# Performance work log

Measured on AMD Instinct MI355X. Metric: run time of the kernel, lower is better.

Reference implementation:

```python
import jax, jax.numpy as jnp
import numpy as np

EMB = 512
GP = 128
NH = 8
HD = EMB // NH  # 64
B = 2
S = 1024


def _rel_shift(x):
    # Faithful port of DoubleAttentionLayer._rel_shift (pads dim 1, reinterprets
    # (B, J+1, K, n) as (J+1, B, K, n), drops first slice). Row-major reshape
    # semantics match torch .view on contiguous tensors exactly.
    Bsz, J, K, N = x.shape
    zp = jnp.zeros((Bsz, 1, K, N), x.dtype)
    xp = jnp.concatenate([zp, x], axis=1).reshape(J + 1, Bsz, K, N)
    return xp[1:].reshape(Bsz, J, K, N)


def _layernorm(x):
    # nn.LayerNorm(emb_dim, elementwise_affine=False), eps=1e-5
    m = jnp.mean(x, axis=-1, keepdims=True)
    v = jnp.var(x, axis=-1, keepdims=True)
    return (x - m) / jnp.sqrt(v + 1e-5)


def _attention(q, k, v, Bc, Bp, gpe, mask, Wp_w, Wp_b):
    Bsz, J, E = q.shape
    K = k.shape[1]
    # content scores
    qc = jnp.tanh((q + Bc).reshape(Bsz, J, NH, HD))
    kh = jnp.tanh(k.reshape(Bsz, K, NH, HD))
    ctx = jnp.einsum('bjnd,bknd->bjkn', qc, kh)
    # position scores (tanh before reshape in source for qp -- elementwise, same math)
    qp = jnp.tanh(q + Bp).reshape(Bsz, J, NH, HD)
    kp = jnp.tanh((gpe @ Wp_w + Wp_b).reshape(Bsz, -1, NH, HD))
    pos = jnp.einsum('bjnd,bknd->bjkn', qp, kp)
    pad = ctx.shape[2] - pos.shape[2]  # static; 0 in this configuration
    if pad > 0:
        # replicate-pad pos at front of k dim; constant(0)-pad mask (torch F.pad defaults)
        pos = jnp.concatenate([jnp.broadcast_to(pos[:, :, :1], (Bsz, J, pad, NH)), pos], axis=2)
        mask = jnp.concatenate([jnp.zeros(mask.shape[:2] + (pad, mask.shape[3]), mask.dtype), mask], axis=2)
    pos = _rel_shift(pos)
    att = (ctx + pos) / (HD ** 0.5) - 1e30 * mask
    att = jax.nn.softmax(att, axis=2)
    vh = jnp.tanh(v.reshape(Bsz, K, NH, HD))
    return jnp.einsum('bjkn,bknd->bjnd', att, vh).reshape(Bsz, J, E)


def setup_inputs() -> dict:
    key = jax.random.key(0)
    ks = jax.random.split(key, 12)
    u_emb = jax.random.normal(ks[0], (B, S, EMB), jnp.float32)
    f_emb = jax.random.normal(ks[1], (B, S, EMB), jnp.float32)
    gpe = jax.random.normal(ks[2], (B, S, GP), jnp.float32)
    # causal masks: 1 where attention is disallowed, broadcast over heads
    causal = (1.0 - jnp.tril(jnp.ones((S, S), jnp.float32)))[None, :, :, None]
    u_mask = jnp.broadcast_to(causal, (B, S, S, 1))
    f_mask = jnp.broadcast_to(causal, (B, S, S, 1))
    w = 0.02
    Wq_w = w * jax.random.normal(ks[3], (EMB, EMB), jnp.float32)
    Wq_b = jnp.zeros((EMB,), jnp.float32)
    Wkv_w = w * jax.random.normal(ks[4], (EMB, 2 * EMB), jnp.float32)
    Wkv_b = jnp.zeros((2 * EMB,), jnp.float32)
    Wp_w = w * jax.random.normal(ks[5], (GP, EMB), jnp.float32)
    Wp_b = jnp.zeros((EMB,), jnp.float32)
    Wu_w = w * jax.random.normal(ks[6], (EMB, EMB), jnp.float32)
    Wu_b = jnp.zeros((EMB,), jnp.float32)
    Bfc = 0.2 * jax.random.normal(ks[7], (1, 1, EMB), jnp.float32)
    Bfp = 0.2 * jax.random.normal(ks[8], (1, 1, EMB), jnp.float32)
    Buc = 0.2 * jax.random.normal(ks[9], (1, 1, EMB), jnp.float32)
    Bup = 0.2 * jax.random.normal(ks[10], (1, 1, EMB), jnp.float32)
    return {"u_emb": u_emb, "f_emb": f_emb, "gpe": gpe, "u_mask": u_mask, "f_mask": f_mask,
            "Wq_w": Wq_w, "Wq_b": Wq_b, "Wkv_w": Wkv_w, "Wkv_b": Wkv_b,
            "Wp_w": Wp_w, "Wp_b": Wp_b, "Wu_w": Wu_w, "Wu_b": Wu_b,
            "Bfc": Bfc, "Bfp": Bfp, "Buc": Buc, "Bup": Bup}


def reference(u_emb, f_emb, gpe, u_mask, f_mask, Wq_w, Wq_b, Wkv_w, Wkv_b,
              Wp_w, Wp_b, Wu_w, Wu_b, Bfc, Bfp, Buc, Bup):
    # first_part=True path: f_mem = f_emb (memory buffer registration has no output effect)
    q_u = f_emb @ Wu_w + Wu_b
    kv = f_emb @ Wkv_w + Wkv_b
    k, v = jnp.split(kv, 2, axis=-1)
    u_out = _layernorm(u_emb + _attention(q_u, k, v, Buc, Bup, gpe, u_mask, Wp_w, Wp_b))
    # last_layer=False: second attention over f stream
    q_f = f_emb @ Wq_w + Wq_b
    f_out = _layernorm(f_emb + _attention(q_f, k, v, Bfc, Bfp, gpe, f_mask, Wp_w, Wp_b))
    return (u_out, f_out)
```

## Files before the change

### kernel.cpp

```cpp
#include <hip/hip_runtime.h>
#include <math.h>

#define EMB 512
#define NH 8
#define HD 64
#define BB 2
#define SS 1024
#define ROWS (BB * SS)

typedef __attribute__((ext_vector_type(8))) short bhalf8;
typedef __attribute__((ext_vector_type(4))) float f32x4;
typedef __attribute__((ext_vector_type(8))) unsigned short us8;
typedef unsigned short ushort_t;

typedef const __attribute__((address_space(1))) void gas_void;
typedef __attribute__((address_space(3))) void las_void;

__device__ __forceinline__ void gl2lds16(const void* g, void* l) {
  __builtin_amdgcn_global_load_lds((gas_void*)g, (las_void*)l, 16, 0, 0);
}

__device__ __forceinline__ unsigned short f2bf(float x) {
  unsigned u = __float_as_uint(x);
  u = (u + 0x7FFFu + ((u >> 16) & 1u)) >> 16;
  return (unsigned short)u;
}
__device__ __forceinline__ float bf2f(unsigned short v) {
  return __uint_as_float(((unsigned)v) << 16);
}
__device__ __forceinline__ float fast_tanh(float x) {
  x = fminf(15.f, fmaxf(-15.f, x));
  const float e = __expf(2.f * x);
  return (e - 1.f) / (e + 1.f);
}

__global__ __launch_bounds__(256) void prep_kernel(
    const float* __restrict__ f_emb, const float* __restrict__ gpe,
    const float* __restrict__ Wu, const float* __restrict__ Wq,
    const float* __restrict__ Wkv, const float* __restrict__ Wp,
    ushort_t* __restrict__ fembB, ushort_t* __restrict__ gpeB,
    ushort_t* __restrict__ WuT, ushort_t* __restrict__ WqT,
    ushort_t* __restrict__ WkvT, ushort_t* __restrict__ WpT,
    float* __restrict__ Onum, float* __restrict__ lpart,
    ushort_t* __restrict__ Qcomb) {
  __shared__ __align__(16) ushort_t sT[64 * 72];
  const int bid = blockIdx.x;
  const int tid = threadIdx.x;

  if (bid < 160) {
    const bool isF = bid < 128;
    const float* src = isF ? f_emb : gpe;
    ushort_t* dst = isF ? fembB : gpeB;
    const size_t base = (size_t)(isF ? bid : bid - 128) * 8192;
#pragma unroll
    for (int j = 0; j < 4; ++j) {
      const size_t off = base + ((size_t)j * 256 + tid) * 8;
      const float4 a = *(const float4*)&src[off];
      const float4 b = *(const float4*)&src[off + 4];
      us8 o;
      o[0] = f2bf(a.x); o[1] = f2bf(a.y); o[2] = f2bf(a.z); o[3] = f2bf(a.w);
      o[4] = f2bf(b.x); o[5] = f2bf(b.y); o[6] = f2bf(b.z); o[7] = f2bf(b.w);
      *(us8*)&dst[off] = o;
    }
  } else if (bid < 432) {
    int t = bid - 160;
    const float* W;
    ushort_t* WT;
    int Nw, Kd, k0, n0;
    if (t < 64) {
      W = Wu; WT = WuT; Nw = 512; Kd = 512;
      k0 = (t >> 3) * 64; n0 = (t & 7) * 64;
    } else if (t < 128) {
      t -= 64; W = Wq; WT = WqT; Nw = 512; Kd = 512;
      k0 = (t >> 3) * 64; n0 = (t & 7) * 64;
    } else if (t < 256) {
      t -= 128; W = Wkv; WT = WkvT; Nw = 1024; Kd = 512;
      k0 = (t >> 4) * 64; n0 = (t & 15) * 64;
    } else {
      t -= 256; W = Wp; WT = WpT; Nw = 512; Kd = 128;
      k0 = (t >> 3) * 64; n0 = (t & 7) * 64;
    }
    const int kk = tid >> 2, seg = tid & 3;
    const float* src = &W[(size_t)(k0 + kk) * Nw + n0 + seg * 16];
    float v[16];
    *(float4*)&v[0] = *(const float4*)&src[0];
    *(float4*)&v[4] = *(const float4*)&src[4];
    *(float4*)&v[8] = *(const float4*)&src[8];
    *(float4*)&v[12] = *(const float4*)&src[12];
#pragma unroll
    for (int i = 0; i < 16; ++i) sT[(seg * 16 + i) * 72 + kk] = f2bf(v[i]);
    __syncthreads();
#pragma unroll
    for (int p = 0; p < 2; ++p) {
      const int idx = p * 256 + tid;
      const int n = idx >> 3, c8 = (idx & 7) * 8;
      const us8 o = *(const us8*)&sT[n * 72 + c8];
      *(us8*)&WT[(size_t)(n0 + n) * Kd + k0 + c8] = o;
    }
  } else if (bid < 688) {
    const float4 z = {0.f, 0.f, 0.f, 0.f};
    const size_t b0 = (size_t)(bid - 432) * 2048;
#pragma unroll
    for (int j = 0; j < 8; ++j) ((float4*)Onum)[b0 + j * 256 + tid] = z;
  } else if (bid < 692) {
    const float4 z = {0.f, 0.f, 0.f, 0.f};
    const size_t b0 = (size_t)(bid - 688) * 2048;
#pragma unroll
    for (int j = 0; j < 8; ++j) ((float4*)lpart)[b0 + j * 256 + tid] = z;
  } else {
    const int t2 = tid >> 7, rem = tid & 127;
    const int h = rem >> 4, d4 = (rem & 15) * 4;
    *(ushort4*)&Qcomb[((size_t)t2 * ROWS + 1023) * 1024 + h * 128 + 64 + d4] =
        make_ushort4(0, 0, 0, 0);
  }
}

__global__ __launch_bounds__(256, 3) void projpe_kernel(
    const ushort_t* __restrict__ fembB, const ushort_t* __restrict__ gpeB,
    const ushort_t* __restrict__ WuT, const ushort_t* __restrict__ WqT,
    const ushort_t* __restrict__ WkvT, const ushort_t* __restrict__ WpT,
    const float* __restrict__ Wu_b, const float* __restrict__ Wq_b,
    const float* __restrict__ Wkv_b, const float* __restrict__ Wp_b,
    const float* __restrict__ Buc, const float* __restrict__ Bup,
    const float* __restrict__ Bfc, const float* __restrict__ Bfp,
    ushort_t* __restrict__ Qcomb, ushort_t* __restrict__ Kcomb,
    ushort_t* __restrict__ vhT) {
  const int bx = blockIdx.x;
  const int mb = blockIdx.y * 128;
  const int tid = threadIdx.x;
  const int w = tid >> 6, lane = tid & 63;
  const int ln = lane & 15, quad = lane >> 4;
  const int wm = (w >> 1) * 64, wn = (w & 1) * 32;

  __shared__ __align__(16) ushort_t sMem[24576];

  const bool isPe = (bx >= 32);
  const int nb = isPe ? 0 : bx * 64;
  const int npbase = isPe ? (bx - 32) * 64 : 0;
  const ushort_t* Asrc = isPe ? gpeB : fembB;
  const int lda = isPe ? 128 : 512;
  const int trips = isPe ? 2 : 8;

  const ushort_t* Wt;
  int Kd, coff;
  if (isPe) { Wt = WpT; Kd = 128; coff = npbase; }
  else if (nb < 512) { Wt = WuT; Kd = 512; coff = nb; }
  else if (nb < 1024) { Wt = WqT; Kd = 512; coff = nb - 512; }
  else { Wt = WkvT; Kd = 512; coff = nb - 1024; }

  const int l3 = lane >> 3, c7 = lane & 7;
  const int swz = (c7 ^ l3) * 8;

#define STAGE_PP(T_, P_)                                                     \
  {                                                                          \
    const int k1_ = (T_) * 64;                                               \
    ushort_t* dA_ = sMem + (P_) * 8192;                                      \
    ushort_t* dB_ = sMem + 16384 + (P_) * 4096;                              \
    _Pragma("unroll") for (int s_ = 0; s_ < 4; ++s_) {                       \
      const int q_ = w * 4 + s_;                                             \
      const int r_ = q_ * 8 + l3;                                            \
      gl2lds16(&Asrc[(size_t)(mb + r_) * lda + k1_ + swz], &dA_[q_ * 512]);  \
    }                                                                        \
    _Pragma("unroll") for (int s_ = 0; s_ < 2; ++s_) {                       \
      const int q_ = w * 2 + s_;                                             \
      const int r_ = q_ * 8 + l3;                                            \
      gl2lds16(&Wt[(size_t)(coff + r_) * Kd + k1_ + swz], &dB_[q_ * 512]);   \
    }                                                                        \
  }

  f32x4 acc[4][2];
#pragma unroll
  for (int rt = 0; rt < 4; ++rt)
#pragma unroll
    for (int ct = 0; ct < 2; ++ct) acc[rt][ct] = (f32x4){0.f, 0.f, 0.f, 0.f};

  STAGE_PP(0, 0);

  for (int t0 = 0; t0 < trips; ++t0) {
    __syncthreads();
    if (t0 < trips - 1) STAGE_PP(t0 + 1, (t0 + 1) & 1);
    const ushort_t* bA = sMem + (t0 & 1) * 8192;
    const ushort_t* bB = sMem + 16384 + (t0 & 1) * 4096;
#pragma unroll
    for (int kc = 0; kc < 2; ++kc) {
      bhalf8 af[4], bfr[2];
#pragma unroll
      for (int rt = 0; rt < 4; ++rt) {
        const int row = wm + rt * 16 + ln;
        af[rt] = *(const bhalf8*)&bA[row * 64 +
                                     (((kc * 4 + quad) ^ (row & 7)) << 3)];
      }
#pragma unroll
      for (int ct = 0; ct < 2; ++ct) {
        const int row = wn + ct * 16 + ln;
        bfr[ct] = *(const bhalf8*)&bB[row * 64 +
                                      (((kc * 4 + quad) ^ (row & 7)) << 3)];
      }
#pragma unroll
      for (int rt = 0; rt < 4; ++rt)
#pragma unroll
        for (int ct = 0; ct < 2; ++ct)
          acc[rt][ct] = __builtin_amdgcn_mfma_f32_16x16x32_bf16(
              af[rt], bfr[ct], acc[rt][ct], 0, 0, 0);
    }
  }

  __syncthreads();
  ushort_t* sOut = sMem;

  if (!isPe && nb >= 1536) {
#pragma unroll
    for (int ct = 0; ct < 2; ++ct) {
      const int nl = wn + ct * 16 + ln;
      const float wb = Wkv_b[nb + nl - 1024];
#pragma unroll
      for (int rt = 0; rt < 4; ++rt)
#pragma unroll
        for (int r = 0; r < 4; ++r) {
          const int ml = wm + rt * 16 + quad * 4 + r;
          sOut[nl * 136 + ml] = f2bf(fast_tanh(acc[rt][ct][r] + wb));
        }
    }
    __syncthreads();
    const int b = mb >> 10, mo = mb & 1023;
#pragma unroll
    for (int i = 0; i < 4; ++i) {
      const int idx = tid + i * 256;
      const int nl = idx >> 4, m8 = (idx & 15) * 8;
      const us8 v = *(const us8*)&sOut[nl * 136 + m8];
      *(us8*)&vhT[((size_t)b * 512 + (nb - 1536) + nl) * 1024 + mo + m8] = v;
    }
  } else {
    const float* WB =
        isPe ? Wp_b : (nb < 512 ? Wu_b : (nb < 1024 ? Wq_b : Wkv_b));
    const int woff =
        isPe ? npbase : (nb < 512 ? nb : (nb < 1024 ? nb - 512 : nb - 1024));
    const bool rawDump = (!isPe && nb < 1024);
#pragma unroll
    for (int ct = 0; ct < 2; ++ct) {
      const int nl = wn + ct * 16 + ln;
      const float wb = WB[woff + nl];
#pragma unroll
      for (int rt = 0; rt < 4; ++rt)
#pragma unroll
        for (int r = 0; r < 4; ++r) {
          const int ml = wm + rt * 16 + quad * 4 + r;
          const float v = acc[rt][ct][r] + wb;
          sOut[ml * 72 + nl] = f2bf(rawDump ? v : fast_tanh(v));
        }
    }
    __syncthreads();
#pragma unroll
    for (int i = 0; i < 4; ++i) {
      const int idx = tid + i * 256;
      const int rr = idx >> 3, c8 = (idx & 7) * 8;
      const int m = mb + rr;
      const us8 v = *(const us8*)&sOut[rr * 72 + c8];
      if (isPe) {
        const int n = npbase + c8;
        const int h = n >> 6;
        *(us8*)&Kcomb[(size_t)m * 1024 + h * 128 + 64 + (n & 63)] = v;
      } else if (nb < 1024) {
        const int strm = nb >= 512 ? 1 : 0;
        const int n = (nb - strm * 512) + c8;
        const int h = n >> 6;
        const float* BC = strm ? Bfc : Buc;
        const float* BP = strm ? Bfp : Bup;
        float bcA[8], bpA[8];
        *(float4*)&bcA[0] = *(const float4*)&BC[n];
        *(float4*)&bcA[4] = *(const float4*)&BC[n + 4];
        *(float4*)&bpA[0] = *(const float4*)&BP[n];
        *(float4*)&bpA[4] = *(const float4*)&BP[n + 4];
        us8 oc, op;
#pragma unroll
        for (int jj = 0; jj < 8; ++jj) {
          const float vv = bf2f((unsigned short)v[jj]);
          oc[jj] = f2bf(fast_tanh(vv + bcA[jj]));
          op[jj] = f2bf(fast_tanh(vv + bpA[jj]));
        }
        *(us8*)&Qcomb[((size_t)strm * ROWS + m) * 1024 + h * 128 + (n & 63)] =
            oc;
        if (m != 0) {
          const int mp = (m < 1024) ? m - 1 : m;
          *(us8*)&Qcomb[((size_t)strm * ROWS + mp) * 1024 + h * 128 + 64 +
                        (n & 63)] = op;
        }
      } else {
        const int n = (nb - 1024) + c8;
        const int h = n >> 6;
        *(us8*)&Kcomb[(size_t)m * 1024 + h * 128 + (n & 63)] = v;
      }
    }
  }
}

__global__ __launch_bounds__(256, 2) void attn_kernel(
    const ushort_t* __restrict__ Qcomb, const ushort_t* __restrict__ Kcomb,
    const ushort_t* __restrict__ vhT, float* __restrict__ Onum,
    float* __restrict__ lpart) {
  const int bid = blockIdx.x;
  const int tid = threadIdx.x;
  const int w = tid >> 6, lane = tid & 63;
  const int ln = lane & 15, quad = lane >> 4;

  __shared__ __align__(16) ushort_t sK[2 * 64 * 128];
  __shared__ __align__(16) ushort_t sV[2 * 64 * 64];
  __shared__ __align__(16) ushort_t sP[64 * 72];

  const int G0 = (bid * 17) >> 1;
  const int G1 = ((bid + 1) * 17) >> 1;
  const int cnt = G1 - G0;

  int c = G0 / 136;
  int u = G0 - c * 136;
  int jt = (int)((sqrtf(8.f * u + 1.f) - 1.f) * 0.5f);
  while ((jt + 1) * (jt + 2) / 2 <= u) ++jt;
  while (jt * (jt + 1) / 2 > u) --jt;
  int kt = u - jt * (jt + 1) / 2;
  int t = c >> 4, b = (c >> 3) & 1, h = c & 7;

  const int l4 = lane >> 4, p15 = lane & 15;
  const int l3 = lane >> 3, l7 = lane & 7;
#define STAGE_KV(B_, H_, KT_, BUF_)                                          \
  {                                                                          \
    const size_t kb_ = ((size_t)(B_)*SS + (KT_)*64) * 1024 + (H_)*128;       \
    ushort_t* bk_ = sK + (BUF_)*8192;                                        \
    _Pragma("unroll") for (int s_ = 0; s_ < 4; ++s_) {                       \
      const int q_ = w * 4 + s_;                                             \
      const int r_ = q_ * 4 + l4;                                            \
      const int gl_ = p15 ^ (r_ & 7);                                        \
      gl2lds16(&Kcomb[kb_ + (size_t)r_ * 1024 + gl_ * 8], &bk_[q_ * 512]);   \
    }                                                                        \
    const size_t vb_ = ((size_t)(B_)*512 + (H_)*64) * 1024 + (KT_)*64;       \
    ushort_t* bv_ = sV + (BUF_)*4096;                                        \
    _Pragma("unroll") for (int s_ = 0; s_ < 2; ++s_) {                       \
      const int q_ = w * 2 + s_;                                             \
      const int r_ = q_ * 8 + l3;                                            \
      const int gl_ = l7 ^ (r_ & 7);                                         \
      gl2lds16(&vhT[vb_ + (size_t)r_ * 1024 + gl_ * 8], &bv_[q_ * 512]);     \
    }                                                                        \
  }

  bhalf8 aq[4];
#define LOAD_AQ(T_, B_, H_, JT_)                                             \
  {                                                                          \
    const size_t qb_ =                                                       \
        ((size_t)(T_)*ROWS + (B_)*SS + (JT_)*64 + w * 16 + ln) * 1024 +      \
        (H_)*128 + quad * 8;                                                 \
    _Pragma("unroll") for (int kc_ = 0; kc_ < 4; ++kc_) aq[kc_] =            \
        *(const bhalf8*)&Qcomb[qb_ + kc_ * 32];                              \
  }

  STAGE_KV(b, h, kt, 0);
  LOAD_AQ(t, b, h, jt);

  f32x4 oacc[4];
#pragma unroll
  for (int ct = 0; ct < 4; ++ct) oacc[ct] = (f32x4){0.f, 0.f, 0.f, 0.f};
  float lsum[4] = {0.f, 0.f, 0.f, 0.f};

  for (int it = 0; it < cnt; ++it) {
    __syncthreads();
    const ushort_t* bK = sK + (it & 1) * 8192;
    const ushort_t* bV = sV + (it & 1) * 4096;

    int c2 = c, jt2 = jt, kt2 = kt + 1;
    if (kt2 > jt) {
      jt2 = jt + 1; kt2 = 0;
      if (jt2 > 15) { c2 = c + 1; jt2 = 0; }
    }
    if (it < cnt - 1) {
      const int b2 = (c2 >> 3) & 1, h2 = c2 & 7;
      STAGE_KV(b2, h2, kt2, ((it + 1) & 1));
    }

    f32x4 sacc[4];
#pragma unroll
    for (int ct = 0; ct < 4; ++ct) {
      sacc[ct] = (f32x4){0.f, 0.f, 0.f, 0.f};
#pragma unroll
      for (int kc = 0; kc < 4; ++kc) {
        const bhalf8 bk = *(const bhalf8*)&bK[(ct * 16 + ln) * 128 +
                                             (((kc * 4 + quad) ^ l7) << 3)];
        sacc[ct] = __builtin_amdgcn_mfma_f32_16x16x32_bf16(aq[kc], bk,
                                                           sacc[ct], 0, 0, 0);
      }
    }

    const bool diag = (kt == jt);
#pragma unroll
    for (int ct = 0; ct < 4; ++ct)
#pragma unroll
      for (int r = 0; r < 4; ++r) {
        float p;
        if (diag && (ct * 16 + ln > w * 16 + quad * 4 + r))
          p = 0.f;
        else
          p = __expf(sacc[ct][r] * 0.125f - 16.f);
        sacc[ct][r] = p;
        lsum[r] += p;
      }

#pragma unroll
    for (int ct = 0; ct < 4; ++ct)
#pragma unroll
      for (int r = 0; r < 4; ++r)
        sP[(w * 16 + quad * 4 + r) * 72 + ct * 16 + ln] =
            (ushort_t)(__float_as_uint(sacc[ct][r]) >> 16);

#pragma unroll
    for (int kc = 0; kc < 2; ++kc) {
      const bhalf8 ap =
          *(const bhalf8*)&sP[(w * 16 + ln) * 72 + kc * 32 + quad * 8];
#pragma unroll
      for (int ct = 0; ct < 4; ++ct) {
        const bhalf8 bv = *(const bhalf8*)&bV[(ct * 16 + ln) * 64 +
                                             (((kc * 4 + quad) ^ l7) << 3)];
        oacc[ct] = __builtin_amdgcn_mfma_f32_16x16x32_bf16(ap, bv, oacc[ct],
                                                           0, 0, 0);
      }
    }

    const bool rowEnd = (it == cnt - 1) || (jt2 != jt) || (c2 != c);
    if (rowEnd) {
#pragma unroll
      for (int r = 0; r < 4; ++r) {
        float s = lsum[r];
        s += __shfl_xor(s, 1);
        s += __shfl_xor(s, 2);
        s += __shfl_xor(s, 4);
        s += __shfl_xor(s, 8);
        const int j = jt * 64 + w * 16 + quad * 4 + r;
        if (ln == 0)
          atomicAdd(&lpart[((((t * 2 + b) << 10) + j) << 3) + h], s);
        const size_t orow = (((size_t)t * ROWS + b * SS + j) << 9) + h * 64;
#pragma unroll
        for (int ct = 0; ct < 4; ++ct)
          atomicAdd(&Onum[orow + ct * 16 + ln], oacc[ct][r]);
        lsum[r] = 0.f;
      }
#pragma unroll
      for (int ct = 0; ct < 4; ++ct) oacc[ct] = (f32x4){0.f, 0.f, 0.f, 0.f};
      if (it < cnt - 1) {
        const int t2 = c2 >> 4, b2 = (c2 >> 3) & 1, h2 = c2 & 7;
        LOAD_AQ(t2, b2, h2, jt2);
      }
    }
    c = c2; jt = jt2; kt = kt2;
    t = c >> 4; b = (c >> 3) & 1; h = c & 7;
  }
}

__global__ __launch_bounds__(256) void ln_kernel(
    const float* __restrict__ u_emb, const float* __restrict__ f_emb,
    const float* __restrict__ Onum, const float* __restrict__ lpart,
    float* __restrict__ out) {
  const int rid = blockIdx.x * 4 + (threadIdx.x >> 6);
  const int lane = threadIdx.x & 63;
  const int t = rid >> 11, row = rid & 2047;
  const int b = row >> 10, j = row & 1023;
  const float* resid = t ? f_emb : u_emb;
  const size_t base = (size_t)row * 512;
  const size_t obase = ((size_t)t * ROWS + row) * 512;
  const int o = lane * 8;
  const int h = lane >> 3;
  const float inv = 1.f / lpart[((((t * 2 + b) << 10) + j) << 3) + h];

  const float4 n0 = *(const float4*)&Onum[obase + o];
  const float4 n1 = *(const float4*)&Onum[obase + o + 4];
  const float4 r0 = *(const float4*)&resid[base + o];
  const float4 r1 = *(const float4*)&resid[base + o + 4];
  float y[8];
  y[0] = r0.x + n0.x * inv; y[1] = r0.y + n0.y * inv;
  y[2] = r0.z + n0.z * inv; y[3] = r0.w + n0.w * inv;
  y[4] = r1.x + n1.x * inv; y[5] = r1.y + n1.y * inv;
  y[6] = r1.z + n1.z * inv; y[7] = r1.w + n1.w * inv;

  float s = 0.f, q = 0.f;
#pragma unroll
  for (int i = 0; i < 8; ++i) {
    s += y[i];
    q += y[i] * y[i];
  }
#pragma unroll
  for (int off = 1; off < 64; off <<= 1) {
    s += __shfl_xor(s, off);
    q += __shfl_xor(q, off);
  }
  const float mean = s * (1.f / 512.f);
  const float var = q * (1.f / 512.f) - mean * mean;
  const float rstd = rsqrtf(var + 1e-5f);

  float4 o0, o1;
  o0.x = (y[0] - mean) * rstd; o0.y = (y[1] - mean) * rstd;
  o0.z = (y[2] - mean) * rstd; o0.w = (y[3] - mean) * rstd;
  o1.x = (y[4] - mean) * rstd; o1.y = (y[5] - mean) * rstd;
  o1.z = (y[6] - mean) * rstd; o1.w = (y[7] - mean) * rstd;
  *(float4*)&out[obase + o] = o0;
  *(float4*)&out[obase + o + 4] = o1;
}

extern "C" void kernel_launch(void* const* d_in, const int* in_sizes, int n_in,
                              void* d_out, int out_size, void* d_ws,
                              size_t ws_size, hipStream_t stream) {
  (void)in_sizes; (void)n_in; (void)out_size; (void)ws_size;
  const float* u_emb = (const float*)d_in[0];
  const float* f_emb = (const float*)d_in[1];
  const float* gpe = (const float*)d_in[2];
  const float* Wq_w = (const float*)d_in[5];
  const float* Wq_b = (const float*)d_in[6];
  const float* Wkv_w = (const float*)d_in[7];
  const float* Wkv_b = (const float*)d_in[8];
  const float* Wp_w = (const float*)d_in[9];
  const float* Wp_b = (const float*)d_in[10];
  const float* Wu_w = (const float*)d_in[11];
  const float* Wu_b = (const float*)d_in[12];
  const float* Bfc = (const float*)d_in[13];
  const float* Bfp = (const float*)d_in[14];
  const float* Buc = (const float*)d_in[15];
  const float* Bup = (const float*)d_in[16];
  float* out = (float*)d_out;

  ushort_t* ws = (ushort_t*)d_ws;
  const size_t SZ = (size_t)ROWS * EMB;
  ushort_t* Qcomb = ws;
  ushort_t* Kcomb = ws + 4 * SZ;
  ushort_t* vhT = ws + 6 * SZ;
  float* Onum = (float*)(ws + 7 * SZ);
  float* lpart = (float*)(ws + 11 * SZ);
  ushort_t* fembB = ws + 12 * SZ;
  ushort_t* gpeB = ws + 13 * SZ;
  ushort_t* WuT = ws + 13 * SZ + SZ / 4;
  ushort_t* WqT = ws + 13 * SZ + SZ / 2;
  ushort_t* WkvT = ws + 13 * SZ + 3 * (SZ / 4);
  ushort_t* WpT = ws + 13 * SZ + 5 * (SZ / 4);

  dim3 blk(256);
  hipLaunchKernelGGL(prep_kernel, dim3(693), blk, 0, stream, f_emb, gpe, Wu_w,
                     Wq_w, Wkv_w, Wp_w, fembB, gpeB, WuT, WqT, WkvT, WpT, Onum,
                     lpart, Qcomb);
  hipLaunchKernelGGL(projpe_kernel, dim3(40, 16), blk, 0, stream, fembB, gpeB,
                     WuT, WqT, WkvT, WpT, Wu_b, Wq_b, Wkv_b, Wp_b, Buc, Bup,
                     Bfc, Bfp, Qcomb, Kcomb, vhT);
  hipLaunchKernelGGL(attn_kernel, dim3(512), blk, 0, stream, Qcomb, Kcomb, vhT,
                     Onum, lpart);
  hipLaunchKernelGGL(ln_kernel, dim3(1024), blk, 0, stream, u_emb, f_emb, Onum,
                     lpart, out);
}
```

Baseline: 152.0 us.

## Pair causal row tiles per block, drop atomics and normalize in-kernel

The attention kernel now gives each 512-thread block one (stream,batch,head) and a pair of query tiles (15-p and p), which balances causal work at 17 tile-steps per block. Eight waves split the 64 key columns into two halves per row group. This replaces the earlier flat split of tiles across blocks. Because each block owns whole output rows, the row sums are combined in shared memory and normalized output is written directly, removing the atomicAdd traffic and the zero-init of the accumulators. In exchange there are fewer blocks (256), an extra barrier per step, and per-wave MFMA work is halved, so occupancy and latency hiding may change.

```diff
diff --git a/kernel.cpp b/kernel.cpp
--- a/kernel.cpp
+++ b/kernel.cpp
@@ -41,7 +41,6 @@
     ushort_t* __restrict__ fembB, ushort_t* __restrict__ gpeB,
     ushort_t* __restrict__ WuT, ushort_t* __restrict__ WqT,
     ushort_t* __restrict__ WkvT, ushort_t* __restrict__ WpT,
-    float* __restrict__ Onum, float* __restrict__ lpart,
     ushort_t* __restrict__ Qcomb) {
   __shared__ __align__(16) ushort_t sT[64 * 72];
   const int bid = blockIdx.x;
@@ -97,16 +96,6 @@
       const us8 o = *(const us8*)&sT[n * 72 + c8];
       *(us8*)&WT[(size_t)(n0 + n) * Kd + k0 + c8] = o;
     }
-  } else if (bid < 688) {
-    const float4 z = {0.f, 0.f, 0.f, 0.f};
-    const size_t b0 = (size_t)(bid - 432) * 2048;
-#pragma unroll
-    for (int j = 0; j < 8; ++j) ((float4*)Onum)[b0 + j * 256 + tid] = z;
-  } else if (bid < 692) {
-    const float4 z = {0.f, 0.f, 0.f, 0.f};
-    const size_t b0 = (size_t)(bid - 688) * 2048;
-#pragma unroll
-    for (int j = 0; j < 8; ++j) ((float4*)lpart)[b0 + j * 256 + tid] = z;
   } else {
     const int t2 = tid >> 7, rem = tid & 127;
     const int h = rem >> 4, d4 = (rem & 15) * 4;
@@ -294,94 +283,82 @@
   }
 }
 
-__global__ __launch_bounds__(256, 2) void attn_kernel(
+__global__ __launch_bounds__(512, 2) void attn_kernel(
     const ushort_t* __restrict__ Qcomb, const ushort_t* __restrict__ Kcomb,
-    const ushort_t* __restrict__ vhT, float* __restrict__ Onum,
-    float* __restrict__ lpart) {
+    const ushort_t* __restrict__ vhT, float* __restrict__ Ofin) {
   const int bid = blockIdx.x;
   const int tid = threadIdx.x;
   const int w = tid >> 6, lane = tid & 63;
   const int ln = lane & 15, quad = lane >> 4;
-
-  __shared__ __align__(16) ushort_t sK[2 * 64 * 128];
-  __shared__ __align__(16) ushort_t sV[2 * 64 * 64];
-  __shared__ __align__(16) ushort_t sP[64 * 72];
-
-  const int G0 = (bid * 17) >> 1;
-  const int G1 = ((bid + 1) * 17) >> 1;
-  const int cnt = G1 - G0;
-
-  int c = G0 / 136;
-  int u = G0 - c * 136;
-  int jt = (int)((sqrtf(8.f * u + 1.f) - 1.f) * 0.5f);
-  while ((jt + 1) * (jt + 2) / 2 <= u) ++jt;
-  while (jt * (jt + 1) / 2 > u) --jt;
-  int kt = u - jt * (jt + 1) / 2;
-  int t = c >> 4, b = (c >> 3) & 1, h = c & 7;
-
+  const int wr = w >> 1, wc = w & 1;
   const int l4 = lane >> 4, p15 = lane & 15;
   const int l3 = lane >> 3, l7 = lane & 7;
-#define STAGE_KV(B_, H_, KT_, BUF_)                                          \
-  {                                                                          \
-    const size_t kb_ = ((size_t)(B_)*SS + (KT_)*64) * 1024 + (H_)*128;       \
-    ushort_t* bk_ = sK + (BUF_)*8192;                                        \
-    _Pragma("unroll") for (int s_ = 0; s_ < 4; ++s_) {                       \
-      const int q_ = w * 4 + s_;                                             \
-      const int r_ = q_ * 4 + l4;                                            \
-      const int gl_ = p15 ^ (r_ & 7);                                        \
-      gl2lds16(&Kcomb[kb_ + (size_t)r_ * 1024 + gl_ * 8], &bk_[q_ * 512]);   \
-    }                                                                        \
-    const size_t vb_ = ((size_t)(B_)*512 + (H_)*64) * 1024 + (KT_)*64;       \
-    ushort_t* bv_ = sV + (BUF_)*4096;                                        \
-    _Pragma("unroll") for (int s_ = 0; s_ < 2; ++s_) {                       \
-      const int q_ = w * 2 + s_;                                             \
-      const int r_ = q_ * 8 + l3;                                            \
-      const int gl_ = l7 ^ (r_ & 7);                                         \
-      gl2lds16(&vhT[vb_ + (size_t)r_ * 1024 + gl_ * 8], &bv_[q_ * 512]);     \
-    }                                                                        \
+
+  __shared__ __align__(16) ushort_t sK[2 * 8192];
+  __shared__ __align__(16) ushort_t sV[2 * 4096];
+  __shared__ __align__(16) ushort_t sP[64 * 72];
+  __shared__ float lsf[2][64];
+
+  const int c = bid >> 3, pi = bid & 7;
+  const int jA = 15 - pi, jB = pi;
+  const int t = c >> 4, b = (c >> 3) & 1, h = c & 7;
+
+#define STAGE_KV(KT_, BUF_)                                                   \
+  {                                                                           \
+    const size_t kb_ = ((size_t)b * SS + (KT_)*64) * 1024 + h * 128;          \
+    ushort_t* bk_ = sK + (BUF_)*8192;                                         \
+    _Pragma("unroll") for (int s_ = 0; s_ < 2; ++s_) {                        \
+      const int q_ = w * 2 + s_;                                              \
+      const int r_ = q_ * 4 + l4;                                             \
+      const int gl_ = p15 ^ (r_ & 7);                                         \
+      gl2lds16(&Kcomb[kb_ + (size_t)r_ * 1024 + gl_ * 8], &bk_[q_ * 512]);    \
+    }                                                                         \
+    const size_t vb_ = ((size_t)b * 512 + h * 64) * 1024 + (KT_)*64;          \
+    ushort_t* bv_ = sV + (BUF_)*4096;                                         \
+    {                                                                         \
+      const int r_ = w * 8 + l3;                                              \
+      const int gl_ = l7 ^ (r_ & 7);                                          \
+      gl2lds16(&vhT[vb_ + (size_t)r_ * 1024 + gl_ * 8], &bv_[w * 512]);       \
+    }                                                                         \
   }
 
   bhalf8 aq[4];
-#define LOAD_AQ(T_, B_, H_, JT_)                                             \
-  {                                                                          \
-    const size_t qb_ =                                                       \
-        ((size_t)(T_)*ROWS + (B_)*SS + (JT_)*64 + w * 16 + ln) * 1024 +      \
-        (H_)*128 + quad * 8;                                                 \
-    _Pragma("unroll") for (int kc_ = 0; kc_ < 4; ++kc_) aq[kc_] =            \
-        *(const bhalf8*)&Qcomb[qb_ + kc_ * 32];                              \
-  }
-
-  STAGE_KV(b, h, kt, 0);
-  LOAD_AQ(t, b, h, jt);
-
-  f32x4 oacc[4];
-#pragma unroll
-  for (int ct = 0; ct < 4; ++ct) oacc[ct] = (f32x4){0.f, 0.f, 0.f, 0.f};
+#define LOAD_AQ(JT_)                                                          \
+  {                                                                           \
+    const size_t qb_ =                                                        \
+        ((size_t)t * ROWS + b * SS + (JT_)*64 + wr * 16 + ln) * 1024 +        \
+        h * 128 + quad * 8;                                                   \
+    _Pragma("unroll") for (int kc_ = 0; kc_ < 4; ++kc_) aq[kc_] =             \
+        *(const bhalf8*)&Qcomb[qb_ + kc_ * 32];                               \
+  }
+
+  STAGE_KV(0, 0);
+  LOAD_AQ(jA);
+
+  f32x4 oacc[2];
+  oacc[0] = (f32x4){0.f, 0.f, 0.f, 0.f};
+  oacc[1] = (f32x4){0.f, 0.f, 0.f, 0.f};
   float lsum[4] = {0.f, 0.f, 0.f, 0.f};
 
-  for (int it = 0; it < cnt; ++it) {
+  int jt = jA, kt = 0;
+  for (int it = 0; it < 17; ++it) {
     __syncthreads();
     const ushort_t* bK = sK + (it & 1) * 8192;
     const ushort_t* bV = sV + (it & 1) * 4096;
 
-    int c2 = c, jt2 = jt, kt2 = kt + 1;
-    if (kt2 > jt) {
-      jt2 = jt + 1; kt2 = 0;
-      if (jt2 > 15) { c2 = c + 1; jt2 = 0; }
-    }
-    if (it < cnt - 1) {
-      const int b2 = (c2 >> 3) & 1, h2 = c2 & 7;
-      STAGE_KV(b2, h2, kt2, ((it + 1) & 1));
-    }
-
-    f32x4 sacc[4];
-#pragma unroll
-    for (int ct = 0; ct < 4; ++ct) {
+    int jt2 = jt, kt2 = kt + 1;
+    if (kt2 > jt) { jt2 = jB; kt2 = 0; }
+    if (it < 16) STAGE_KV(kt2, ((it + 1) & 1));
+
+    f32x4 sacc[2];
+#pragma unroll
+    for (int ct = 0; ct < 2; ++ct) {
       sacc[ct] = (f32x4){0.f, 0.f, 0.f, 0.f};
 #pragma unroll
       for (int kc = 0; kc < 4; ++kc) {
-        const bhalf8 bk = *(const bhalf8*)&bK[(ct * 16 + ln) * 128 +
-                                             (((kc * 4 + quad) ^ l7) << 3)];
+        const bhalf8 bk =
+            *(const bhalf8*)&bK[(wc * 32 + ct * 16 + ln) * 128 +
+                                (((kc * 4 + quad) ^ l7) << 3)];
         sacc[ct] = __builtin_amdgcn_mfma_f32_16x16x32_bf16(aq[kc], bk,
                                                            sacc[ct], 0, 0, 0);
       }
@@ -389,11 +366,11 @@
 
     const bool diag = (kt == jt);
 #pragma unroll
-    for (int ct = 0; ct < 4; ++ct)
+    for (int ct = 0; ct < 2; ++ct)
 #pragma unroll
       for (int r = 0; r < 4; ++r) {
         float p;
-        if (diag && (ct * 16 + ln > w * 16 + quad * 4 + r))
+        if (diag && (wc * 32 + ct * 16 + ln > wr * 16 + quad * 4 + r))
           p = 0.f;
         else
           p = __expf(sacc[ct][r] * 0.125f - 16.f);
@@ -402,27 +379,31 @@
       }
 
 #pragma unroll
-    for (int ct = 0; ct < 4; ++ct)
+    for (int ct = 0; ct < 2; ++ct)
 #pragma unroll
       for (int r = 0; r < 4; ++r)
-        sP[(w * 16 + quad * 4 + r) * 72 + ct * 16 + ln] =
+        sP[(wr * 16 + quad * 4 + r) * 72 + wc * 32 + ct * 16 + ln] =
             (ushort_t)(__float_as_uint(sacc[ct][r]) >> 16);
+
+    asm volatile("s_waitcnt lgkmcnt(0)" ::: "memory");
+    __builtin_amdgcn_s_barrier();
+    __builtin_amdgcn_sched_barrier(0);
 
 #pragma unroll
     for (int kc = 0; kc < 2; ++kc) {
       const bhalf8 ap =
-          *(const bhalf8*)&sP[(w * 16 + ln) * 72 + kc * 32 + quad * 8];
-#pragma unroll
-      for (int ct = 0; ct < 4; ++ct) {
-        const bhalf8 bv = *(const bhalf8*)&bV[(ct * 16 + ln) * 64 +
-                                             (((kc * 4 + quad) ^ l7) << 3)];
+          *(const bhalf8*)&sP[(wr * 16 + ln) * 72 + kc * 32 + quad * 8];
+#pragma unroll
+      for (int ct = 0; ct < 2; ++ct) {
+        const bhalf8 bv =
+            *(const bhalf8*)&bV[(wc * 32 + ct * 16 + ln) * 64 +
+                                (((kc * 4 + quad) ^ l7) << 3)];
         oacc[ct] = __builtin_amdgcn_mfma_f32_16x16x32_bf16(ap, bv, oacc[ct],
                                                            0, 0, 0);
       }
     }
 
-    const bool rowEnd = (it == cnt - 1) || (jt2 != jt) || (c2 != c);
-    if (rowEnd) {
+    if (kt == jt) {
 #pragma unroll
       for (int r = 0; r < 4; ++r) {
         float s = lsum[r];
@@ -430,51 +411,48 @@
         s += __shfl_xor(s, 2);
         s += __shfl_xor(s, 4);
         s += __shfl_xor(s, 8);
-        const int j = jt * 64 + w * 16 + quad * 4 + r;
-        if (ln == 0)
-          atomicAdd(&lpart[((((t * 2 + b) << 10) + j) << 3) + h], s);
+        if (ln == 0) lsf[wc][wr * 16 + quad * 4 + r] = s;
+      }
+      __syncthreads();
+#pragma unroll
+      for (int r = 0; r < 4; ++r) {
+        const int rl = wr * 16 + quad * 4 + r;
+        const float rinv = 1.f / (lsf[0][rl] + lsf[1][rl]);
+        const int j = jt * 64 + rl;
         const size_t orow = (((size_t)t * ROWS + b * SS + j) << 9) + h * 64;
 #pragma unroll
-        for (int ct = 0; ct < 4; ++ct)
-          atomicAdd(&Onum[orow + ct * 16 + ln], oacc[ct][r]);
+        for (int ct = 0; ct < 2; ++ct)
+          Ofin[orow + wc * 32 + ct * 16 + ln] = oacc[ct][r] * rinv;
         lsum[r] = 0.f;
       }
-#pragma unroll
-      for (int ct = 0; ct < 4; ++ct) oacc[ct] = (f32x4){0.f, 0.f, 0.f, 0.f};
-      if (it < cnt - 1) {
-        const int t2 = c2 >> 4, b2 = (c2 >> 3) & 1, h2 = c2 & 7;
-        LOAD_AQ(t2, b2, h2, jt2);
-      }
-    }
-    c = c2; jt = jt2; kt = kt2;
-    t = c >> 4; b = (c >> 3) & 1; h = c & 7;
+      oacc[0] = (f32x4){0.f, 0.f, 0.f, 0.f};
+      oacc[1] = (f32x4){0.f, 0.f, 0.f, 0.f};
+      if (jt == jA) LOAD_AQ(jB);
+    }
+    jt = jt2; kt = kt2;
   }
 }
 
 __global__ __launch_bounds__(256) void ln_kernel(
     const float* __restrict__ u_emb, const float* __restrict__ f_emb,
-    const float* __restrict__ Onum, const float* __restrict__ lpart,
-    float* __restrict__ out) {
+    const float* __restrict__ Ofin, float* __restrict__ out) {
   const int rid = blockIdx.x * 4 + (threadIdx.x >> 6);
   const int lane = threadIdx.x & 63;
   const int t = rid >> 11, row = rid & 2047;
-  const int b = row >> 10, j = row & 1023;
   const float* resid = t ? f_emb : u_emb;
   const size_t base = (size_t)row * 512;
   const size_t obase = ((size_t)t * ROWS + row) * 512;
   const int o = lane * 8;
-  const int h = lane >> 3;
-  const float inv = 1.f / lpart[((((t * 2 + b) << 10) + j) << 3) + h];
-
-  const float4 n0 = *(const float4*)&Onum[obase + o];
-  const float4 n1 = *(const float4*)&Onum[obase + o + 4];
+
+  const float4 n0 = *(const float4*)&Ofin[obase + o];
+  const float4 n1 = *(const float4*)&Ofin[obase + o + 4];
   const float4 r0 = *(const float4*)&resid[base + o];
   const float4 r1 = *(const float4*)&resid[base + o + 4];
   float y[8];
-  y[0] = r0.x + n0.x * inv; y[1] = r0.y + n0.y * inv;
-  y[2] = r0.z + n0.z * inv; y[3] = r0.w + n0.w * inv;
-  y[4] = r1.x + n1.x * inv; y[5] = r1.y + n1.y * inv;
-  y[6] = r1.z + n1.z * inv; y[7] = r1.w + n1.w * inv;
+  y[0] = r0.x + n0.x; y[1] = r0.y + n0.y;
+  y[2] = r0.z + n0.z; y[3] = r0.w + n0.w;
+  y[4] = r1.x + n1.x; y[5] = r1.y + n1.y;
+  y[6] = r1.z + n1.z; y[7] = r1.w + n1.w;
 
   float s = 0.f, q = 0.f;
 #pragma unroll
@@ -526,8 +504,7 @@
   ushort_t* Qcomb = ws;
   ushort_t* Kcomb = ws + 4 * SZ;
   ushort_t* vhT = ws + 6 * SZ;
-  float* Onum = (float*)(ws + 7 * SZ);
-  float* lpart = (float*)(ws + 11 * SZ);
+  float* Ofin = (float*)(ws + 7 * SZ);
   ushort_t* fembB = ws + 12 * SZ;
   ushort_t* gpeB = ws + 13 * SZ;
   ushort_t* WuT = ws + 13 * SZ + SZ / 4;
@@ -536,14 +513,14 @@
   ushort_t* WpT = ws + 13 * SZ + 5 * (SZ / 4);
 
   dim3 blk(256);
-  hipLaunchKernelGGL(prep_kernel, dim3(693), blk, 0, stream, f_emb, gpe, Wu_w,
-                     Wq_w, Wkv_w, Wp_w, fembB, gpeB, WuT, WqT, WkvT, WpT, Onum,
-                     lpart, Qcomb);
+  hipLaunchKernelGGL(prep_kernel, dim3(433), blk, 0, stream, f_emb, gpe, Wu_w,
+                     Wq_w, Wkv_w, Wp_w, fembB, gpeB, WuT, WqT, WkvT, WpT,
+                     Qcomb);
   hipLaunchKernelGGL(projpe_kernel, dim3(40, 16), blk, 0, stream, fembB, gpeB,
                      WuT, WqT, WkvT, WpT, Wu_b, Wq_b, Wkv_b, Wp_b, Buc, Bup,
                      Bfc, Bfp, Qcomb, Kcomb, vhT);
-  hipLaunchKernelGGL(attn_kernel, dim3(512), blk, 0, stream, Qcomb, Kcomb, vhT,
-                     Onum, lpart);
-  hipLaunchKernelGGL(ln_kernel, dim3(1024), blk, 0, stream, u_emb, f_emb, Onum,
-                     lpart, out);
-}
+  hipLaunchKernelGGL(attn_kernel, dim3(256), dim3(512), 0, stream, Qcomb,
+                     Kcomb, vhT, Ofin);
+  hipLaunchKernelGGL(ln_kernel, dim3(1024), blk, 0, stream, u_emb, f_emb,
+                     Ofin, out);
+}
```

Result: faster. 148.2 us (-2.5%).
